# Kernel tuning notes

Hardware: AMD Instinct MI355X
Metric: run time of the kernel (lower is better)

## Reference

```python
import jax, jax.numpy as jnp
import numpy as np

MEAN = np.array([0.485, 0.456, 0.406], np.float32).reshape(1, 3, 1, 1)
STD = np.array([0.229, 0.224, 0.225], np.float32).reshape(1, 3, 1, 1)
BN_EPS = 1e-5


def _srm_kernels():
    """Standard SRM 30-filter 5x5 high-pass bank (Fridrich) -> [30,1,5,5]."""
    ks = []
    Z = lambda: np.zeros((5, 5), np.float32)
    D8 = [(-1, 0), (-1, 1), (0, 1), (1, 1), (1, 0), (1, -1), (0, -1), (-1, -1)]
    for dy, dx in D8:  # 8 first-order
        k = Z(); k[2, 2] = -1.0; k[2 + dy, 2 + dx] = 1.0; ks.append(k)
    for dy, dx in D8[:4]:  # 4 second-order
        k = Z(); k[2, 2] = -2.0; k[2 + dy, 2 + dx] = 1.0; k[2 - dy, 2 - dx] = 1.0
        ks.append(k / 2.0)
    for dy, dx in D8:  # 8 third-order
        k = Z()
        k[2 - dy, 2 - dx] = -1.0; k[2, 2] = 3.0
        k[2 + dy, 2 + dx] = -3.0; k[2 + 2 * dy, 2 + 2 * dx] = 1.0
        ks.append(k / 3.0)
    sq3 = np.array([[-1, 2, -1], [2, -4, 2], [-1, 2, -1]], np.float32) / 4.0
    k = Z(); k[1:4, 1:4] = sq3; ks.append(k)  # SQUARE 3x3
    sq5 = np.array([[-1, 2, -2, 2, -1], [2, -6, 8, -6, 2], [-2, 8, -12, 8, -2],
                    [2, -6, 8, -6, 2], [-1, 2, -2, 2, -1]], np.float32) / 12.0
    ks.append(sq5)  # SQUARE 5x5
    e3 = np.array([[-1, 2, -1], [2, -4, 2], [0, 0, 0]], np.float32) / 4.0
    for r in range(4):  # 4 EDGE 3x3
        k = Z(); k[1:4, 1:4] = np.rot90(e3, r); ks.append(k)
    e5 = np.array([[-1, 2, -2, 2, -1], [2, -6, 8, -6, 2], [-2, 8, -12, 8, -2],
                   [0, 0, 0, 0, 0], [0, 0, 0, 0, 0]], np.float32) / 4.0
    for r in range(4):  # 4 EDGE 5x5
        ks.append(np.rot90(e5, r).copy())
    return np.stack(ks)[:, None]  # [30,1,5,5]

SRM_K = jnp.asarray(_srm_kernels())
GAUSS_K = jnp.asarray((np.outer([1, 4, 6, 4, 1], [1, 4, 6, 4, 1]) / 256.0)
                      .astype(np.float32))[None, None]  # [1,1,5,5]
CFA_K = jnp.asarray((np.array([[0, 1, 0], [1, 0, 1], [0, 1, 0]], np.float32) / 4.0))[None, None]


def conv2d(x, w, b=None):
    y = jax.lax.conv_general_dilated(x, w, (1, 1), 'SAME',
                                     dimension_numbers=('NCHW', 'OIHW', 'NCHW'))
    if b is not None:
        y = y + b[None, :, None, None]
    return y


def batchnorm(x, g, b, m, v):
    inv = jax.lax.rsqrt(v + BN_EPS)
    return (x - m[None, :, None, None]) * (g * inv)[None, :, None, None] + b[None, :, None, None]


def extract_features(x):
    """Batched PRNU(1) + SRM(30) + CFA(1) feature maps -> [B,32,H,W]."""
    img = jnp.clip(x * STD + MEAN, 0.0, 1.0)  # denormalize
    gray = (0.299 * img[:, 0] + 0.587 * img[:, 1] + 0.114 * img[:, 2])[:, None]  # [B,1,H,W]
    prnu = gray - conv2d(gray, GAUSS_K)            # denoise-subtract noise residual
    srm = conv2d(gray, SRM_K)                       # [B,30,H,W]
    green = img[:, 1:2]
    cfa = green - conv2d(green, CFA_K)              # CFA interpolation residual
    return jnp.concatenate([prnu, srm, cfa], axis=1)  # [B,32,H,W]


def setup_inputs() -> dict:
    key = jax.random.key(0)
    ks = jax.random.split(key, 16)
    B, H, W = 16, 256, 256
    d = {"x": jax.random.normal(ks[0], (B, 3, H, W), jnp.float32)}
    cins = [32, 64, 64, 64]
    for i in range(4):
        cin, co = cins[i], 64
        scale = (2.0 / (cin * 9)) ** 0.5  # kaiming
        d[f"w{i+1}"] = jax.random.normal(ks[1 + i], (co, cin, 3, 3), jnp.float32) * scale
        d[f"b{i+1}"] = jnp.zeros((co,), jnp.float32)
        d[f"g{i+1}"] = jnp.ones((co,), jnp.float32)
        d[f"be{i+1}"] = jnp.zeros((co,), jnp.float32)
        d[f"m{i+1}"] = jax.random.normal(ks[5 + i], (co,), jnp.float32) * 0.1
        d[f"v{i+1}"] = jax.random.uniform(ks[9 + i], (co,), jnp.float32, 0.5, 1.5)
    return d


def reference(x, w1, b1, g1, be1, m1, v1, w2, b2, g2, be2, m2, v2,
              w3, b3, g3, be3, m3, v3, w4, b4, g4, be4, m4, v4):
    h = extract_features(x)
    for w, b, g, be, m, v in ((w1, b1, g1, be1, m1, v1), (w2, b2, g2, be2, m2, v2),
                              (w3, b3, g3, be3, m3, v3), (w4, b4, g4, be4, m4, v4)):
        h = jax.nn.relu(batchnorm(conv2d(h, w, b), g, be, m, v))
    return h  # [B,64,H,W]
```

## Files before the change

### kernel.cpp

```cpp
#include <hip/hip_runtime.h>
#include <hip/hip_bf16.h>
#include <cstddef>

#define B_ 16
#define H_ 256
#define W_ 256
#define HW_ (H_ * W_)
#define P_ 258


typedef _Float16 half8 __attribute__((ext_vector_type(8)));
typedef float floatx4 __attribute__((ext_vector_type(4)));

__device__ __forceinline__ void gload_lds16(void* lds, const void* g) {
  __builtin_amdgcn_global_load_lds(
      (const __attribute__((address_space(1))) unsigned int*)g,
      (__attribute__((address_space(3))) unsigned int*)lds, 16, 0, 0);
}

__global__ __launch_bounds__(256) void zero_border3(_Float16* __restrict__ f,
                                                    _Float16* __restrict__ a,
                                                    _Float16* __restrict__ bb) {
  int idx = blockIdx.x * 256 + threadIdx.x;
  int total = 16 * 20 * 1028;
  if (idx >= total) return;
  int p = idx % 1028;
  int rest = idx / 1028;
  int cg = rest % 20;
  int b = rest / 20;
  _Float16* buf;
  int ncg, c;
  if (cg < 4) { buf = f; ncg = 4; c = cg; }
  else if (cg < 12) { buf = a; ncg = 8; c = cg - 4; }
  else { buf = bb; ncg = 8; c = cg - 12; }
  int row, col;
  if (p < 258) { row = 0; col = p; }
  else if (p < 516) { row = 257; col = p - 258; }
  else if (p < 772) { row = p - 515; col = 0; }
  else { row = p - 771; col = 257; }
  *(floatx4*)&buf[(((size_t)(b * ncg + c) * P_ + row) * P_ + col) * 8] =
      (floatx4)0.f;
}

__global__ __launch_bounds__(256) void feat_kernel(const float* __restrict__ x,
                                                   _Float16* __restrict__ F) {
  __shared__ float sg[36][37];
  __shared__ float sgr[36][37];

  const int b = blockIdx.z;
  const int y0 = blockIdx.y * 32;
  const int x0 = blockIdx.x * 32;
  const float* xb = x + (size_t)b * 3 * HW_;

  for (int i = threadIdx.x; i < 36 * 36; i += 256) {
    int iy = i / 36, ix = i % 36;
    int gy = y0 + iy - 2, gx = x0 + ix - 2;
    float gray = 0.f, green = 0.f;
    if (gy >= 0 && gy < H_ && gx >= 0 && gx < W_) {
      int idx = gy * W_ + gx;
      float r = fminf(fmaxf(xb[idx] * 0.229f + 0.485f, 0.f), 1.f);
      float g = fminf(fmaxf(xb[idx + HW_] * 0.224f + 0.456f, 0.f), 1.f);
      float bl = fminf(fmaxf(xb[idx + 2 * HW_] * 0.225f + 0.406f, 0.f), 1.f);
      gray = 0.299f * r + 0.587f * g + 0.114f * bl;
      green = g;
    }
    sg[iy][ix] = gray;
    sgr[iy][ix] = green;
  }
  __syncthreads();

  for (int p = threadIdx.x; p < 32 * 32; p += 256) {
    const int py = p >> 5, px = p & 31;
    const int ly = py + 2, lx = px + 2;
#define G(dy, dx) sg[ly + (dy)][lx + (dx)]
    float f[32];
    const float c = G(0, 0);

    {
      const float ga[5] = {1.f, 4.f, 6.f, 4.f, 1.f};
      float s = 0.f;
#pragma unroll
      for (int i = 0; i < 5; i++) {
        float rs = 0.f;
#pragma unroll
        for (int j = 0; j < 5; j++) rs += ga[j] * G(i - 2, j - 2);
        s += ga[i] * rs;
      }
      f[0] = c - s * (1.0f / 256.0f);
    }

    const int dy8[8] = {-1, -1, 0, 1, 1, 1, 0, -1};
    const int dx8[8] = {0, 1, 1, 1, 0, -1, -1, -1};

#pragma unroll
    for (int k = 0; k < 8; k++) f[1 + k] = G(dy8[k], dx8[k]) - c;
#pragma unroll
    for (int k = 0; k < 4; k++)
      f[9 + k] = 0.5f * (G(dy8[k], dx8[k]) + G(-dy8[k], -dx8[k])) - c;
#pragma unroll
    for (int k = 0; k < 8; k++)
      f[13 + k] = (-G(-dy8[k], -dx8[k]) + 3.f * c - 3.f * G(dy8[k], dx8[k]) +
                   G(2 * dy8[k], 2 * dx8[k])) * (1.f / 3.f);

    {
      const float sq3[3][3] = {{-1, 2, -1}, {2, -4, 2}, {-1, 2, -1}};
      float s = 0.f;
#pragma unroll
      for (int i = 0; i < 3; i++)
#pragma unroll
        for (int j = 0; j < 3; j++) s += sq3[i][j] * G(i - 1, j - 1);
      f[21] = s * 0.25f;
    }
    {
      const float sq5[5][5] = {{-1, 2, -2, 2, -1},
                               {2, -6, 8, -6, 2},
                               {-2, 8, -12, 8, -2},
                               {2, -6, 8, -6, 2},
                               {-1, 2, -2, 2, -1}};
      float s = 0.f;
#pragma unroll
      for (int i = 0; i < 5; i++)
#pragma unroll
        for (int j = 0; j < 5; j++) s += sq5[i][j] * G(i - 2, j - 2);
      f[22] = s * (1.0f / 12.0f);
    }
    {
      const float e3[3][3] = {{-1, 2, -1}, {2, -4, 2}, {0, 0, 0}};
      float s0 = 0.f, s1 = 0.f, s2 = 0.f, s3 = 0.f;
#pragma unroll
      for (int i = 0; i < 3; i++)
#pragma unroll
        for (int j = 0; j < 3; j++) {
          float v = G(i - 1, j - 1);
          s0 += e3[i][j] * v;
          s1 += e3[j][2 - i] * v;
          s2 += e3[2 - i][2 - j] * v;
          s3 += e3[2 - j][i] * v;
        }
      f[23] = s0 * 0.25f;
      f[24] = s1 * 0.25f;
      f[25] = s2 * 0.25f;
      f[26] = s3 * 0.25f;
    }
    {
      const float e5[5][5] = {{-1, 2, -2, 2, -1},
                              {2, -6, 8, -6, 2},
                              {-2, 8, -12, 8, -2},
                              {0, 0, 0, 0, 0},
                              {0, 0, 0, 0, 0}};
      float s0 = 0.f, s1 = 0.f, s2 = 0.f, s3 = 0.f;
#pragma unroll
      for (int i = 0; i < 5; i++)
#pragma unroll
        for (int j = 0; j < 5; j++) {
          float v = G(i - 2, j - 2);
          s0 += e5[i][j] * v;
          s1 += e5[j][4 - i] * v;
          s2 += e5[4 - i][4 - j] * v;
          s3 += e5[4 - j][i] * v;
        }
      f[27] = s0 * 0.25f;
      f[28] = s1 * 0.25f;
      f[29] = s2 * 0.25f;
      f[30] = s3 * 0.25f;
    }
    {
      float gc = sgr[ly][lx];
      f[31] = gc - 0.25f * (sgr[ly - 1][lx] + sgr[ly][lx - 1] +
                            sgr[ly][lx + 1] + sgr[ly + 1][lx]);
    }
#undef G

    _Float16 h[32];
#pragma unroll
    for (int cc = 0; cc < 32; cc++) h[cc] = (_Float16)f[cc];
    const floatx4* src = (const floatx4*)h;
#pragma unroll
    for (int cg = 0; cg < 4; cg++)
      *(floatx4*)&F[(((size_t)(b * 4 + cg) * P_ + (y0 + py + 1)) * P_ +
                     (x0 + px + 1)) * 8] = src[cg];
  }
}

__global__ void wprep4_kernel(
    const float* __restrict__ w1, const float* __restrict__ b1,
    const float* __restrict__ g1, const float* __restrict__ be1,
    const float* __restrict__ m1, const float* __restrict__ v1,
    const float* __restrict__ w2, const float* __restrict__ b2,
    const float* __restrict__ g2, const float* __restrict__ be2,
    const float* __restrict__ m2, const float* __restrict__ v2,
    const float* __restrict__ w3, const float* __restrict__ b3,
    const float* __restrict__ g3, const float* __restrict__ be3,
    const float* __restrict__ m3, const float* __restrict__ v3,
    const float* __restrict__ w4, const float* __restrict__ b4,
    const float* __restrict__ g4, const float* __restrict__ be4,
    const float* __restrict__ m4, const float* __restrict__ v4,
    _Float16* __restrict__ wp1, _Float16* __restrict__ wp2,
    _Float16* __restrict__ wp3, _Float16* __restrict__ wp4,
    float* __restrict__ scsh) {
  const int layer = blockIdx.y;
  const float *w, *bias, *g, *be, *m, *v;
  _Float16* wp;
  int cin;
  switch (layer) {
    case 0: w = w1; bias = b1; g = g1; be = be1; m = m1; v = v1; wp = wp1; cin = 32; break;
    case 1: w = w2; bias = b2; g = g2; be = be2; m = m2; v = v2; wp = wp2; cin = 64; break;
    case 2: w = w3; bias = b3; g = g3; be = be3; m = m3; v = v3; wp = wp3; cin = 64; break;
    default: w = w4; bias = b4; g = g4; be = be4; m = m4; v = v4; wp = wp4; cin = 64; break;
  }
  int i = blockIdx.x * 256 + threadIdx.x;
  int total = cin * 9 * 64;
  if (i < total) {
    int j = i & 7;
    int co = (i >> 3) & 63;
    int rest = i >> 9;
    int t = rest % 9;
    int qc = rest / 9;
    int ci = qc * 8 + j;
    wp[i] = (_Float16)w[((size_t)co * cin + ci) * 9 + t];
  }
  if (i < 64) {
    float s = g[i] * rsqrtf(v[i] + 1e-5f);
    scsh[layer * 128 + i] = s;
    scsh[layer * 128 + 64 + i] = be[i] + (bias[i] - m[i]) * s;
  }
}

template <int CIN, bool FINAL>
__global__ __launch_bounds__(256, 2) void conv_mfma(
    const _Float16* __restrict__ in, const _Float16* __restrict__ wp,
    const float* __restrict__ sc, const float* __restrict__ sh,
    void* __restrict__ outv) {
  __shared__ char smem[42240 + 36864];
  _Float16(*s_in)[10][66][8] = (_Float16(*)[10][66][8])smem;
  _Float16(*s_w)[9][64][8] = (_Float16(*)[9][64][8])(smem + 42240);

  const int bid = blockIdx.x;
  const int sid = (bid & 7) * 256 + (bid >> 3);
  const int b = sid >> 7;
  const int y0 = ((sid >> 2) & 31) * 8;
  const int x0 = (sid & 3) * 64;

  const int tid = threadIdx.x;
  const int wid = tid >> 6;
  const int lane = tid & 63;
  const int quad = lane >> 4;
  const int ln = lane & 15;

  floatx4 acc[8][4];
#pragma unroll
  for (int mt = 0; mt < 8; mt++)
#pragma unroll
    for (int nt = 0; nt < 4; nt++) acc[mt][nt] = (floatx4)0.f;

  for (int kc = 0; kc < CIN / 32; kc++) {
    __syncthreads();
    for (int i = tid; i < 2640; i += 256) {
      int q = i / 660, rem = i % 660;
      int row = rem / 66, col = rem % 66;
      gload_lds16(smem + i * 16,
                  &in[(((size_t)(b * (CIN / 8) + kc * 4 + q) * P_ +
                        (y0 + row)) * P_ + (x0 + col)) * 8]);
    }
    for (int i = tid; i < 2304; i += 256) {
      gload_lds16(smem + 42240 + i * 16, wp + ((size_t)kc * 2304 + i) * 8);
    }
    __syncthreads();

#pragma unroll
    for (int t = 0; t < 9; t++) {
      const int ty = t / 3, tx = t % 3;
      half8 a[8], bb[4];
#pragma unroll
      for (int nt = 0; nt < 4; nt++)
        bb[nt] = *(const half8*)&s_w[quad][t][nt * 16 + ln][0];
#pragma unroll
      for (int mt = 0; mt < 8; mt++)
        a[mt] = *(const half8*)
            &s_in[quad][2 * wid + ty + (mt >> 2)][(mt & 3) * 16 + ln + tx][0];
#pragma unroll
      for (int mt = 0; mt < 8; mt++)
#pragma unroll
        for (int nt = 0; nt < 4; nt++)
          acc[mt][nt] = __builtin_amdgcn_mfma_f32_16x16x32_f16(
              a[mt], bb[nt], acc[mt][nt], 0, 0, 0);
    }
  }

  if (FINAL) {
    float* out = (float*)outv;
#pragma unroll
    for (int nt = 0; nt < 4; nt++) {
      int co = nt * 16 + ln;
      float s = sc[co], t0 = sh[co];
#pragma unroll
      for (int mt = 0; mt < 8; mt++) {
        int y = y0 + 2 * wid + (mt >> 2);
        int xb = x0 + (mt & 3) * 16 + quad * 4;
        floatx4 vv;
#pragma unroll
        for (int r = 0; r < 4; r++) vv[r] = fmaxf(acc[mt][nt][r] * s + t0, 0.f);
        *(floatx4*)&out[(((size_t)b * 64 + co) * H_ + y) * W_ + xb] = vv;
      }
    }
  } else {
    __syncthreads();
    _Float16* s_out = (_Float16*)smem + wid * 8192;
#pragma unroll
    for (int nt = 0; nt < 4; nt++) {
      int co = nt * 16 + ln;
      float s = sc[co], t0 = sh[co];
      int cog = co >> 3, clo = co & 7;
#pragma unroll
      for (int mt = 0; mt < 8; mt++) {
        int pix0 = (mt >> 2) * 64 + (mt & 3) * 16 + quad * 4;
#pragma unroll
        for (int r = 0; r < 4; r++) {
          int pix = pix0 + r;
          s_out[pix * 64 + (((cog ^ (pix & 7)) << 3) | clo)] =
              (_Float16)fmaxf(acc[mt][nt][r] * s + t0, 0.f);
        }
      }
    }
    asm volatile("s_waitcnt lgkmcnt(0)" ::: "memory");
    _Float16* out = (_Float16*)outv;
#pragma unroll
    for (int k = 0; k < 16; k++) {
      int rw = k >> 3, cog = k & 7;
      int pix = rw * 64 + lane;
      int gy = y0 + 2 * wid + rw + 1, gx = x0 + lane + 1;
      *(floatx4*)&out[(((size_t)(b * 8 + cog) * P_ + gy) * P_ + gx) * 8] =
          *(const floatx4*)&s_out[pix * 64 + ((cog ^ (lane & 7)) << 3)];
    }
  }
}

extern "C" void kernel_launch(void* const* d_in, const int* in_sizes, int n_in,
                              void* d_out, int out_size, void* d_ws,
                              size_t ws_size, hipStream_t stream) {
  const float* x = (const float*)d_in[0];
#define LAYER_PTRS(i)                                                       \
  const float* w##i = (const float*)d_in[1 + ((i)-1) * 6 + 0];              \
  const float* b##i = (const float*)d_in[1 + ((i)-1) * 6 + 1];              \
  const float* g##i = (const float*)d_in[1 + ((i)-1) * 6 + 2];              \
  const float* be##i = (const float*)d_in[1 + ((i)-1) * 6 + 3];             \
  const float* m##i = (const float*)d_in[1 + ((i)-1) * 6 + 4];              \
  const float* v##i = (const float*)d_in[1 + ((i)-1) * 6 + 5];
  LAYER_PTRS(1)
  LAYER_PTRS(2)
  LAYER_PTRS(3)
  LAYER_PTRS(4)
#undef LAYER_PTRS

  char* ws = (char*)d_ws;
  const size_t featB = (size_t)16 * 4 * P_ * P_ * 8 * 2;
  const size_t actB64 = (size_t)16 * 8 * P_ * P_ * 8 * 2;
  _Float16* feat = (_Float16*)ws;
  _Float16* actA = (_Float16*)(ws + featB);
  _Float16* actB = (_Float16*)(ws + featB + actB64);
  char* wbase = ws + featB + 2 * actB64;
  _Float16* wp1 = (_Float16*)(wbase);
  _Float16* wp2 = (_Float16*)(wbase + 36864);
  _Float16* wp3 = (_Float16*)(wbase + 36864 + 73728);
  _Float16* wp4 = (_Float16*)(wbase + 36864 + 2 * 73728);
  float* scsh = (float*)(wbase + 36864 + 3 * 73728);
  float *sc1 = scsh, *sh1 = scsh + 64;
  float *sc2 = scsh + 128, *sh2 = scsh + 192;
  float *sc3 = scsh + 256, *sh3 = scsh + 320;
  float *sc4 = scsh + 384, *sh4 = scsh + 448;

  dim3 wgrid(144, 4);
  wprep4_kernel<<<wgrid, 256, 0, stream>>>(
      w1, b1, g1, be1, m1, v1, w2, b2, g2, be2, m2, v2,
      w3, b3, g3, be3, m3, v3, w4, b4, g4, be4, m4, v4,
      wp1, wp2, wp3, wp4, scsh);

  zero_border3<<<1285, 256, 0, stream>>>(feat, actA, actB);

  dim3 fgrid(W_ / 32, H_ / 32, B_);
  feat_kernel<<<fgrid, 256, 0, stream>>>(x, feat);

  conv_mfma<32, false><<<2048, 256, 0, stream>>>(feat, wp1, sc1, sh1, actA);
  conv_mfma<64, false><<<2048, 256, 0, stream>>>(actA, wp2, sc2, sh2, actB);
  conv_mfma<64, false><<<2048, 256, 0, stream>>>(actB, wp3, sc3, sh3, actA);
  conv_mfma<64, true><<<2048, 256, 0, stream>>>(actA, wp4, sc4, sh4, d_out);
}
```

Before: 624.6 us.

## Add producer-consumer warp-specialized conv kernel for 64-channel layers

```diff
diff --git a/kernel.cpp b/kernel.cpp
--- a/kernel.cpp
+++ b/kernel.cpp
@@ -335,6 +335,137 @@
   }
 }
 
+template <bool FINAL>
+__global__ __launch_bounds__(384, 1) void conv_pc(
+    const _Float16* __restrict__ in, const _Float16* __restrict__ wp,
+    const float* __restrict__ sc, const float* __restrict__ sh,
+    void* __restrict__ outv) {
+  constexpr int BUF = 79104;
+  __shared__ char smem[2 * BUF];
+
+  const int bid = blockIdx.x;
+  const int sid = (bid & 7) * 256 + (bid >> 3);
+  const int b = sid >> 7;
+  const int y0 = ((sid >> 2) & 31) * 8;
+  const int x0 = (sid & 3) * 64;
+
+  const int tid = threadIdx.x;
+  const int wid = tid >> 6;
+  const bool producer = wid >= 4;
+  const int lane = tid & 63;
+  const int quad = lane >> 4;
+  const int ln = lane & 15;
+
+  floatx4 acc[8][4];
+#pragma unroll
+  for (int mt = 0; mt < 8; mt++)
+#pragma unroll
+    for (int nt = 0; nt < 4; nt++) acc[mt][nt] = (floatx4)0.f;
+
+  auto stage = [&](int bufidx, int kcn) {
+    char* dst = smem + bufidx * BUF;
+    const int pt = tid - 256;
+    for (int i = pt; i < 2640; i += 128) {
+      int q = i / 660, rem = i % 660;
+      int row = rem / 66, col = rem % 66;
+      gload_lds16(dst + i * 16,
+                  &in[(((size_t)(b * 8 + kcn * 4 + q) * P_ + (y0 + row)) * P_ +
+                       (x0 + col)) * 8]);
+    }
+    for (int i = pt; i < 2304; i += 128) {
+      gload_lds16(dst + 42240 + i * 16, wp + ((size_t)kcn * 2304 + i) * 8);
+    }
+  };
+
+  if (producer) {
+    stage(0, 0);
+    asm volatile("s_waitcnt vmcnt(0)" ::: "memory");
+  }
+  __syncthreads();
+
+  for (int kc = 0; kc < 2; kc++) {
+    if (producer) {
+      if (kc == 0) {
+        stage(1, 1);
+        asm volatile("s_waitcnt vmcnt(0)" ::: "memory");
+      }
+    } else {
+      char* buf = smem + (kc & 1) * BUF;
+      _Float16(*s_in)[10][66][8] = (_Float16(*)[10][66][8])buf;
+      _Float16(*s_w)[9][64][8] = (_Float16(*)[9][64][8])(buf + 42240);
+      __builtin_amdgcn_s_setprio(1);
+#pragma unroll
+      for (int t = 0; t < 9; t++) {
+        const int ty = t / 3, tx = t % 3;
+        half8 a[8], bb[4];
+#pragma unroll
+        for (int nt = 0; nt < 4; nt++)
+          bb[nt] = *(const half8*)&s_w[quad][t][nt * 16 + ln][0];
+#pragma unroll
+        for (int mt = 0; mt < 8; mt++)
+          a[mt] = *(const half8*)
+              &s_in[quad][2 * wid + ty + (mt >> 2)][(mt & 3) * 16 + ln + tx][0];
+#pragma unroll
+        for (int mt = 0; mt < 8; mt++)
+#pragma unroll
+          for (int nt = 0; nt < 4; nt++)
+            acc[mt][nt] = __builtin_amdgcn_mfma_f32_16x16x32_f16(
+                a[mt], bb[nt], acc[mt][nt], 0, 0, 0);
+      }
+      __builtin_amdgcn_s_setprio(0);
+    }
+    __syncthreads();
+  }
+
+  if (producer) return;
+
+  if (FINAL) {
+    float* out = (float*)outv;
+#pragma unroll
+    for (int nt = 0; nt < 4; nt++) {
+      int co = nt * 16 + ln;
+      float s = sc[co], t0 = sh[co];
+#pragma unroll
+      for (int mt = 0; mt < 8; mt++) {
+        int y = y0 + 2 * wid + (mt >> 2);
+        int xb = x0 + (mt & 3) * 16 + quad * 4;
+        floatx4 vv;
+#pragma unroll
+        for (int r = 0; r < 4; r++) vv[r] = fmaxf(acc[mt][nt][r] * s + t0, 0.f);
+        *(floatx4*)&out[(((size_t)b * 64 + co) * H_ + y) * W_ + xb] = vv;
+      }
+    }
+  } else {
+    _Float16* s_out = (_Float16*)smem + wid * 8192;
+#pragma unroll
+    for (int nt = 0; nt < 4; nt++) {
+      int co = nt * 16 + ln;
+      float s = sc[co], t0 = sh[co];
+      int cog = co >> 3, clo = co & 7;
+#pragma unroll
+      for (int mt = 0; mt < 8; mt++) {
+        int pix0 = (mt >> 2) * 64 + (mt & 3) * 16 + quad * 4;
+#pragma unroll
+        for (int r = 0; r < 4; r++) {
+          int pix = pix0 + r;
+          s_out[pix * 64 + (((cog ^ (pix & 7)) << 3) | clo)] =
+              (_Float16)fmaxf(acc[mt][nt][r] * s + t0, 0.f);
+        }
+      }
+    }
+    asm volatile("s_waitcnt lgkmcnt(0)" ::: "memory");
+    _Float16* out = (_Float16*)outv;
+#pragma unroll
+    for (int k = 0; k < 16; k++) {
+      int rw = k >> 3, cog = k & 7;
+      int pix = rw * 64 + lane;
+      int gy = y0 + 2 * wid + rw + 1, gx = x0 + lane + 1;
+      *(floatx4*)&out[(((size_t)(b * 8 + cog) * P_ + gy) * P_ + gx) * 8] =
+          *(const floatx4*)&s_out[pix * 64 + ((cog ^ (lane & 7)) << 3)];
+    }
+  }
+}
+
 extern "C" void kernel_launch(void* const* d_in, const int* in_sizes, int n_in,
                               void* d_out, int out_size, void* d_ws,
                               size_t ws_size, hipStream_t stream) {
@@ -381,7 +512,7 @@
   feat_kernel<<<fgrid, 256, 0, stream>>>(x, feat);
 
   conv_mfma<32, false><<<2048, 256, 0, stream>>>(feat, wp1, sc1, sh1, actA);
-  conv_mfma<64, false><<<2048, 256, 0, stream>>>(actA, wp2, sc2, sh2, actB);
-  conv_mfma<64, false><<<2048, 256, 0, stream>>>(actB, wp3, sc3, sh3, actA);
-  conv_mfma<64, true><<<2048, 256, 0, stream>>>(actA, wp4, sc4, sh4, d_out);
-}
+  conv_pc<false><<<2048, 384, 0, stream>>>(actA, wp2, sc2, sh2, actB);
+  conv_pc<false><<<2048, 384, 0, stream>>>(actB, wp3, sc3, sh3, actA);
+  conv_pc<true><<<2048, 384, 0, stream>>>(actA, wp4, sc4, sh4, d_out);
+}
```

After: 704.5 us. +12.8%, slower.
